# Kernel tuning notes

Measured on AMD Instinct MI355X. Metric: run time of the kernel, lower is better.

The kernel has to match this reference:

```python
import jax, jax.numpy as jnp
import numpy as np

NUM_HEADS = 16

def _apply_rope(t, cos, sin):
    # t: [B, nh, S, hd]; cos/sin: [S, hd//2]
    t1 = t[..., 0::2]
    t2 = t[..., 1::2]
    c = cos[None, None, :, :]
    s = sin[None, None, :, :]
    r1 = t1 * c - t2 * s
    r2 = t1 * s + t2 * c
    # interleave back to [..., hd]
    out = jnp.stack([r1, r2], axis=-1)
    return out.reshape(t.shape)

def setup_inputs() -> dict:
    key = jax.random.key(0)
    ks = jax.random.split(key, 6)
    B, S, H = 1, 4096, 1024
    hd = H // NUM_HEADS
    x = jax.random.normal(ks[0], (B, S, H), dtype=jnp.float32)
    # RoPE angle matrix: theta[pos, i] = pos / 10000^(2i/hd), shape [context, hd//2]
    pos = jnp.arange(S, dtype=jnp.float32)[:, None]
    inv_freq = 1.0 / (10000.0 ** (jnp.arange(0, hd, 2, dtype=jnp.float32) / hd))
    rotation = pos * inv_freq[None, :]
    sc = 1.0 / np.sqrt(H)
    W_qkv = jax.random.normal(ks[1], (H, 3 * H), dtype=jnp.float32) * sc
    b_qkv = jax.random.normal(ks[2], (3 * H,), dtype=jnp.float32) * 0.01
    W_out = jax.random.normal(ks[3], (H, H), dtype=jnp.float32) * sc
    b_out = jax.random.normal(ks[4], (H,), dtype=jnp.float32) * 0.01
    return {"x": x, "rotation": rotation, "W_qkv": W_qkv, "b_qkv": b_qkv,
            "W_out": W_out, "b_out": b_out, "window_size": 33}

def reference(x, rotation, W_qkv, b_qkv, W_out, b_out, window_size):
    B, S, H = x.shape
    nh = NUM_HEADS
    hd = H // nh
    W = window_size
    pad = W // 2
    qkv = x @ W_qkv + b_qkv                               # [B, S, 3H]
    qkv = qkv.reshape(B, S, nh, 3 * hd).transpose(0, 2, 1, 3)  # [B, nh, S, 3hd]
    q, k, v = jnp.split(qkv, 3, axis=-1)                  # each [B, nh, S, hd]
    cos = jnp.cos(rotation[:S])
    sin = jnp.sin(rotation[:S])
    q = _apply_rope(q, cos, sin)
    k = _apply_rope(k, cos, sin)
    # zero-pad along sequence, then gather sliding windows
    k_pad = jnp.pad(k, ((0, 0), (0, 0), (pad, pad), (0, 0)))
    v_pad = jnp.pad(v, ((0, 0), (0, 0), (pad, pad), (0, 0)))
    idx = jnp.arange(S)[:, None] + jnp.arange(W)[None, :]  # [S, W]
    k_win = k_pad[:, :, idx, :]                            # [B, nh, S, W, hd]
    v_win = v_pad[:, :, idx, :]
    scores = jnp.einsum('bnsh,bnswh->bnsw', q, k_win) / np.sqrt(hd)
    attn = jax.nn.softmax(scores, axis=-1)
    ctx = jnp.einsum('bnsw,bnswh->bnsh', attn, v_win)      # [B, nh, S, hd]
    ctx = ctx.transpose(0, 2, 1, 3).reshape(B, S, H)
    return ctx @ W_out + b_out
```

## Files before the change

kernel.cpp:

```cpp
#include <hip/hip_runtime.h>
#include <hip/hip_bf16.h>

#define S_LEN 4096
#define NH 16
#define HD 64
#define WIN 33
#define PAD 16
#define QT 64
#define KROWS 96
#define KPITCH_U 36

typedef short short8 __attribute__((ext_vector_type(8)));
typedef float f32x4 __attribute__((ext_vector_type(4)));

__device__ __forceinline__ float bl(unsigned u){ return __uint_as_float(u << 16); }
__device__ __forceinline__ float bh(unsigned u){ return __uint_as_float(u & 0xffff0000u); }
__device__ __forceinline__ unsigned f2bfu(float f){
  unsigned u = __float_as_uint(f);
  return (u + 0x7fffu + ((u >> 16) & 1u)) >> 16;
}
__device__ __forceinline__ unsigned pack2(float a, float b){ return f2bfu(a) | (f2bfu(b) << 16); }

__device__ __forceinline__ void gload_lds16(const void* g, void* l){
  __builtin_amdgcn_global_load_lds(
      (const __attribute__((address_space(1))) void*)g,
      (__attribute__((address_space(3))) void*)l, 16, 0, 0);
}


__global__ __launch_bounds__(256) void prep_all(
    const float* __restrict__ rot, float2* __restrict__ csq,
    const float* __restrict__ x, __hip_bfloat16* __restrict__ xb,
    const float* __restrict__ Wq, __hip_bfloat16* __restrict__ Wt1,
    const float* __restrict__ Wo, __hip_bfloat16* __restrict__ Wt2)
{
  __shared__ float tile[32][33];
  const int b = blockIdx.x, tid = threadIdx.x;
  if (b < 512) {
    int t = b * 256 + tid;
    float v = rot[t], sv, cv;
    __sincosf(v, &sv, &cv);
    csq[t] = make_float2(cv, sv);
  } else if (b < 2560) {
    int t = (b - 512) * 256 + tid;
    const float4* p = (const float4*)x + (size_t)t * 2;
    float4 a = p[0], c = p[1];
    uint4 o;
    o.x = pack2(a.x, a.y); o.y = pack2(a.z, a.w);
    o.z = pack2(c.x, c.y); o.w = pack2(c.z, c.w);
    ((uint4*)xb)[t] = o;
  } else {
    const float* in; unsigned short* out; int R, C, bx, by;
    if (b < 5632) { int bb = b - 2560; in = Wq; out = (unsigned short*)Wt1; R = 1024; C = 3072; bx = bb % 96; by = bb / 96; }
    else          { int bb = b - 5632; in = Wo; out = (unsigned short*)Wt2; R = 1024; C = 1024; bx = bb % 32; by = bb / 32; }
    int c0 = bx * 32, r0 = by * 32;
    int tx = tid & 31, ty = tid >> 5;
    #pragma unroll
    for (int i = 0; i < 4; ++i) {
      int r = ty + i * 8;
      tile[r][tx] = in[(size_t)(r0 + r) * C + c0 + tx];
    }
    __syncthreads();
    #pragma unroll
    for (int i = 0; i < 4; ++i) {
      int cc = ty + i * 8;
      out[(size_t)(c0 + cc) * R + r0 + tx] = (unsigned short)f2bfu(tile[tx][cc]);
    }
  }
}


__global__ __launch_bounds__(256, 4) void gemm_qkv_rope(
    const __hip_bfloat16* __restrict__ A,
    const __hip_bfloat16* __restrict__ Bt,
    const float* __restrict__ bias,
    const float2* __restrict__ csq,
    unsigned short* __restrict__ Cout,
    int M, int N, int K)
{
  __shared__ unsigned int lA[128 * 64 / 2];
  __shared__ unsigned int lB[96 * 64 / 2];
  const int tid = threadIdx.x;
  const int wave = tid >> 6, lane = tid & 63;
  const int m0 = blockIdx.y * 128, n0 = blockIdx.x * 96;
  const int wm = (wave >> 1) * 64, wn = (wave & 1) * 48;
  const int l16 = lane >> 4, l15 = lane & 15;

  f32x4 acc[4][3];
  #pragma unroll
  for (int i = 0; i < 4; ++i)
    #pragma unroll
    for (int j = 0; j < 3; ++j) acc[i][j] = (f32x4){0.f, 0.f, 0.f, 0.f};

  const int nkt = K / 64;
  for (int kt = 0; kt < nkt; ++kt) {
    __syncthreads();
    #pragma unroll
    for (int it = 0; it < 4; ++it) {
      const int c = it * 256 + tid;
      const int r = c >> 3, s8 = c & 7;
      const int ss = s8 ^ (r & 7);
      gload_lds16(A + (size_t)(m0 + r) * K + kt * 64 + ss * 8, (char*)lA + c * 16);
    }
    #pragma unroll
    for (int it = 0; it < 3; ++it) {
      const int c = it * 256 + tid;
      const int r = c >> 3, s8 = c & 7;
      const int ss = s8 ^ (r & 7);
      gload_lds16(Bt + (size_t)(n0 + r) * K + kt * 64 + ss * 8, (char*)lB + c * 16);
    }
    __syncthreads();
    #pragma unroll
    for (int ks = 0; ks < 2; ++ks) {
      short8 af[4], bfr[3];
      #pragma unroll
      for (int mi = 0; mi < 4; ++mi) {
        const int r = wm + mi * 16 + l15;
        const int slot = (ks * 4 + l16) ^ (r & 7);
        uint4 u = *(const uint4*)((const char*)lA + r * 128 + slot * 16);
        af[mi] = __builtin_bit_cast(short8, u);
      }
      #pragma unroll
      for (int ni = 0; ni < 3; ++ni) {
        const int r = wn + ni * 16 + l15;
        const int slot = (ks * 4 + l16) ^ (r & 7);
        uint4 u = *(const uint4*)((const char*)lB + r * 128 + slot * 16);
        bfr[ni] = __builtin_bit_cast(short8, u);
      }
      #pragma unroll
      for (int mi = 0; mi < 4; ++mi)
        #pragma unroll
        for (int ni = 0; ni < 3; ++ni)
          acc[mi][ni] = __builtin_amdgcn_mfma_f32_16x16x32_bf16(af[mi], bfr[ni], acc[mi][ni], 0, 0, 0);
    }
  }

  #pragma unroll
  for (int ni = 0; ni < 3; ++ni) {
    const int cn = n0 + wn + ni * 16 + l15;
    const int rseg = cn % 192;
    const float bv = bias[cn];
    if (rseg < 128) {
      const int i = (rseg & 63) >> 1;
      const float sgn = (cn & 1) ? 1.f : -1.f;
      #pragma unroll
      for (int mi = 0; mi < 4; ++mi) {
        #pragma unroll
        for (int j = 0; j < 4; ++j) {
          const int rm = m0 + wm + mi * 16 + l16 * 4 + j;
          const float v = acc[mi][ni][j] + bv;
          const float p = __shfl_xor(v, 1);
          const float2 cs = csq[rm * 32 + i];
          Cout[(size_t)rm * N + cn] = (unsigned short)f2bfu(v * cs.x + p * (sgn * cs.y));
        }
      }
    } else {
      #pragma unroll
      for (int mi = 0; mi < 4; ++mi) {
        #pragma unroll
        for (int j = 0; j < 4; ++j) {
          const int rm = m0 + wm + mi * 16 + l16 * 4 + j;
          Cout[(size_t)rm * N + cn] = (unsigned short)f2bfu(acc[mi][ni][j] + bv);
        }
      }
    }
  }
}


__global__ __launch_bounds__(256) void gemm_out(
    const __hip_bfloat16* __restrict__ A,
    const __hip_bfloat16* __restrict__ Bt,
    const float* __restrict__ bias,
    float* __restrict__ Cout,
    int M, int N, int K)
{
  __shared__ unsigned int lA[2][128 * 64 / 2];
  __shared__ unsigned int lB[2][64 * 64 / 2];
  const int tid = threadIdx.x;
  const int wave = tid >> 6, lane = tid & 63;
  const int m0 = blockIdx.y * 128, n0 = blockIdx.x * 64;
  const int wm = (wave >> 1) * 64, wn = (wave & 1) * 32;
  const int l16 = lane >> 4, l15 = lane & 15;

  f32x4 acc[4][2];
  #pragma unroll
  for (int i = 0; i < 4; ++i)
    #pragma unroll
    for (int j = 0; j < 2; ++j) acc[i][j] = (f32x4){0.f, 0.f, 0.f, 0.f};

  auto stage = [&](int buf, int kt) {
    #pragma unroll
    for (int it = 0; it < 4; ++it) {
      const int c = it * 256 + wave * 64 + lane;
      const int r = c >> 3, s8 = c & 7;
      const int ss = s8 ^ (r & 7);
      gload_lds16(A + (size_t)(m0 + r) * K + kt * 64 + ss * 8,
                  (char*)lA[buf] + (it * 256 + wave * 64) * 16);
    }
    #pragma unroll
    for (int it = 0; it < 2; ++it) {
      const int c = it * 256 + wave * 64 + lane;
      const int r = c >> 3, s8 = c & 7;
      const int ss = s8 ^ (r & 7);
      gload_lds16(Bt + (size_t)(n0 + r) * K + kt * 64 + ss * 8,
                  (char*)lB[buf] + (it * 256 + wave * 64) * 16);
    }
  };

  const int nkt = K / 64;
  stage(0, 0);
  int cur = 0;
  for (int kt = 0; kt < nkt; ++kt) {
    const bool pf = (kt + 1 < nkt);
    if (pf) stage(cur ^ 1, kt + 1);
    if (pf) asm volatile("s_waitcnt vmcnt(6)" ::: "memory");
    else    asm volatile("s_waitcnt vmcnt(0)" ::: "memory");
    __builtin_amdgcn_s_barrier();
    __builtin_amdgcn_sched_barrier(0);
    #pragma unroll
    for (int ks = 0; ks < 2; ++ks) {
      short8 af[4], bfr[2];
      #pragma unroll
      for (int mi = 0; mi < 4; ++mi) {
        const int r = wm + mi * 16 + l15;
        const int slot = (ks * 4 + l16) ^ (r & 7);
        uint4 u = *(const uint4*)((const char*)lA[cur] + r * 128 + slot * 16);
        af[mi] = __builtin_bit_cast(short8, u);
      }
      #pragma unroll
      for (int ni = 0; ni < 2; ++ni) {
        const int r = wn + ni * 16 + l15;
        const int slot = (ks * 4 + l16) ^ (r & 7);
        uint4 u = *(const uint4*)((const char*)lB[cur] + r * 128 + slot * 16);
        bfr[ni] = __builtin_bit_cast(short8, u);
      }
      __builtin_amdgcn_s_setprio(1);
      #pragma unroll
      for (int mi = 0; mi < 4; ++mi)
        #pragma unroll
        for (int ni = 0; ni < 2; ++ni)
          acc[mi][ni] = __builtin_amdgcn_mfma_f32_16x16x32_bf16(af[mi], bfr[ni], acc[mi][ni], 0, 0, 0);
      __builtin_amdgcn_s_setprio(0);
    }
    __builtin_amdgcn_sched_barrier(0);
    __builtin_amdgcn_s_barrier();
    cur ^= 1;
  }

  #pragma unroll
  for (int ni = 0; ni < 2; ++ni) {
    const int cn = n0 + wn + ni * 16 + l15;
    const float bv = bias[cn];
    #pragma unroll
    for (int mi = 0; mi < 4; ++mi) {
      #pragma unroll
      for (int j = 0; j < 4; ++j) {
        const int rm = m0 + wm + mi * 16 + l16 * 4 + j;
        Cout[(size_t)rm * N + cn] = acc[mi][ni][j] + bv;
      }
    }
  }
}


__global__ __launch_bounds__(256) void attn_kernel(const __hip_bfloat16* __restrict__ qkv,
                                                   __hip_bfloat16* __restrict__ ctx){
  __shared__ unsigned int kbuf[KROWS * KPITCH_U];
  __shared__ unsigned int vbuf[KROWS * KPITCH_U];
  const int tid = threadIdx.x;
  const int h   = blockIdx.x & 15;
  const int qs0 = (blockIdx.x >> 4) * QT;

  #pragma unroll
  for (int it = 0; it < 3; ++it) {
    int c = tid + it * 256;
    int r = c >> 3, s8 = c & 7;
    int srow = qs0 - PAD + r;
    uint4 kv = make_uint4(0, 0, 0, 0), vv = make_uint4(0, 0, 0, 0);
    if ((unsigned)srow < (unsigned)S_LEN) {
      kv = ((const uint4*)(qkv + (size_t)srow * 3072 + h * 192 + 64))[s8];
      vv = ((const uint4*)(qkv + (size_t)srow * 3072 + h * 192 + 128))[s8];
    }
    *(uint4*)(kbuf + r * KPITCH_U + s8 * 4) = kv;
    *(uint4*)(vbuf + r * KPITCH_U + s8 * 4) = vv;
  }

  const int ql = tid >> 2, t4 = tid & 3;
  const uint4* qp = (const uint4*)(qkv + (size_t)(qs0 + ql) * 3072 + h * 192);
  float qf[64];
  #pragma unroll
  for (int c = 0; c < 8; ++c) {
    uint4 v = qp[c];
    qf[c*8+0] = bl(v.x); qf[c*8+1] = bh(v.x);
    qf[c*8+2] = bl(v.y); qf[c*8+3] = bh(v.y);
    qf[c*8+4] = bl(v.z); qf[c*8+5] = bh(v.z);
    qf[c*8+6] = bl(v.w); qf[c*8+7] = bh(v.w);
  }
  __syncthreads();

  float sc[9];
  #pragma unroll
  for (int j = 0; j < 9; ++j) sc[j] = 0.f;
  float mx = -1e30f;
  #pragma unroll
  for (int j = 0; j < 9; ++j) {
    int w = t4 + 4 * j;
    if (w < WIN) {
      int rw = ql + w;
      const uint4* kp = (const uint4*)(kbuf + rw * KPITCH_U);
      float d = 0.f;
      #pragma unroll
      for (int c = 0; c < 8; ++c) {
        uint4 kv = kp[c];
        d += qf[c*8+0]*bl(kv.x) + qf[c*8+1]*bh(kv.x)
           + qf[c*8+2]*bl(kv.y) + qf[c*8+3]*bh(kv.y)
           + qf[c*8+4]*bl(kv.z) + qf[c*8+5]*bh(kv.z)
           + qf[c*8+6]*bl(kv.w) + qf[c*8+7]*bh(kv.w);
      }
      sc[j] = d * 0.125f;
      mx = fmaxf(mx, sc[j]);
    }
  }
  mx = fmaxf(mx, __shfl_xor(mx, 1));
  mx = fmaxf(mx, __shfl_xor(mx, 2));
  float sum = 0.f;
  #pragma unroll
  for (int j = 0; j < 9; ++j) {
    int w = t4 + 4 * j;
    if (w < WIN) { sc[j] = __expf(sc[j] - mx); sum += sc[j]; }
  }
  sum += __shfl_xor(sum, 1);
  sum += __shfl_xor(sum, 2);
  const float inv = 1.0f / sum;
  #pragma unroll
  for (int j = 0; j < 9; ++j) sc[j] *= inv;

  float accd[16];
  #pragma unroll
  for (int i = 0; i < 16; ++i) accd[i] = 0.f;
  #pragma unroll
  for (int w = 0; w < WIN; ++w) {
    float wgt = __shfl(sc[w >> 2], ((tid & 63) & ~3) | (w & 3), 64);
    int rw = ql + w;
    const uint4* vp = (const uint4*)(vbuf + rw * KPITCH_U + t4 * 8);
    uint4 a = vp[0], b = vp[1];
    float vf[16];
    vf[0]=bl(a.x); vf[1]=bh(a.x); vf[2]=bl(a.y); vf[3]=bh(a.y);
    vf[4]=bl(a.z); vf[5]=bh(a.z); vf[6]=bl(a.w); vf[7]=bh(a.w);
    vf[8]=bl(b.x); vf[9]=bh(b.x); vf[10]=bl(b.y); vf[11]=bh(b.y);
    vf[12]=bl(b.z); vf[13]=bh(b.z); vf[14]=bl(b.w); vf[15]=bh(b.w);
    #pragma unroll
    for (int i = 0; i < 16; ++i) accd[i] += wgt * vf[i];
  }

  unsigned short* op = (unsigned short*)ctx + (size_t)(qs0 + ql) * 1024 + h * 64 + t4 * 16;
  uint4 o1, o2;
  o1.x = pack2(accd[0], accd[1]);  o1.y = pack2(accd[2], accd[3]);
  o1.z = pack2(accd[4], accd[5]);  o1.w = pack2(accd[6], accd[7]);
  o2.x = pack2(accd[8], accd[9]);  o2.y = pack2(accd[10], accd[11]);
  o2.z = pack2(accd[12], accd[13]); o2.w = pack2(accd[14], accd[15]);
  *(uint4*)op = o1;
  *((uint4*)op + 1) = o2;
}


extern "C" void kernel_launch(void* const* d_in, const int* in_sizes, int n_in,
                              void* d_out, int out_size, void* d_ws, size_t ws_size,
                              hipStream_t stream)
{
  const float* x     = (const float*)d_in[0];
  const float* rot   = (const float*)d_in[1];
  const float* W_qkv = (const float*)d_in[2];
  const float* b_qkv = (const float*)d_in[3];
  const float* W_out = (const float*)d_in[4];
  const float* b_out = (const float*)d_in[5];
  float* out = (float*)d_out;

  char* ws = (char*)d_ws;
  __hip_bfloat16* xb   = (__hip_bfloat16*)(ws + 0);
  __hip_bfloat16* Wt1  = (__hip_bfloat16*)(ws + 8388608);
  __hip_bfloat16* Wt2  = (__hip_bfloat16*)(ws + 14680064);
  __hip_bfloat16* qkvb = (__hip_bfloat16*)(ws + 16777216);
  __hip_bfloat16* ctx  = (__hip_bfloat16*)(ws + 41943040);
  float2* csq          = (float2*)(ws + 50331648);

  prep_all<<<6656, 256, 0, stream>>>(rot, csq, x, xb, W_qkv, Wt1, W_out, Wt2);
  gemm_qkv_rope<<<dim3(3072 / 96, 4096 / 128), 256, 0, stream>>>(xb, Wt1, b_qkv, csq,
                                                                 (unsigned short*)qkvb, 4096, 3072, 1024);
  attn_kernel<<<64 * 16, 256, 0, stream>>>(qkvb, ctx);
  gemm_out<<<dim3(1024 / 64, 4096 / 128), 256, 0, stream>>>(ctx, Wt2, b_out, out, 4096, 1024, 1024);
}
```

Measured before the change: 87.95 us.

## Split-K output GEMM with atomic accumulation and bias prefill in prep kernel

The output projection GEMM now splits K in two across a third grid dimension, doubling block count from 512 to 1024, and accumulates partial results into the output with float atomicAdd. The bias is written into the output buffer beforehand by extra blocks in the prep kernel. To fit higher occupancy the LDS double-buffering and priority hints are removed in favour of a simple single-buffer loop. Atomics add memory traffic and make the summation order nondeterministic, and the dropped prefetch may expose load latency.

```diff
diff --git a/kernel.cpp b/kernel.cpp
--- a/kernel.cpp
+++ b/kernel.cpp
@@ -32,7 +32,8 @@
     const float* __restrict__ rot, float2* __restrict__ csq,
     const float* __restrict__ x, __hip_bfloat16* __restrict__ xb,
     const float* __restrict__ Wq, __hip_bfloat16* __restrict__ Wt1,
-    const float* __restrict__ Wo, __hip_bfloat16* __restrict__ Wt2)
+    const float* __restrict__ Wo, __hip_bfloat16* __restrict__ Wt2,
+    const float* __restrict__ b_out, float* __restrict__ out)
 {
   __shared__ float tile[32][33];
   const int b = blockIdx.x, tid = threadIdx.x;
@@ -49,10 +50,10 @@
     o.x = pack2(a.x, a.y); o.y = pack2(a.z, a.w);
     o.z = pack2(c.x, c.y); o.w = pack2(c.z, c.w);
     ((uint4*)xb)[t] = o;
-  } else {
-    const float* in; unsigned short* out; int R, C, bx, by;
-    if (b < 5632) { int bb = b - 2560; in = Wq; out = (unsigned short*)Wt1; R = 1024; C = 3072; bx = bb % 96; by = bb / 96; }
-    else          { int bb = b - 5632; in = Wo; out = (unsigned short*)Wt2; R = 1024; C = 1024; bx = bb % 32; by = bb / 32; }
+  } else if (b < 6656) {
+    const float* in; unsigned short* outp; int R, C, bx, by;
+    if (b < 5632) { int bb = b - 2560; in = Wq; outp = (unsigned short*)Wt1; R = 1024; C = 3072; bx = bb % 96; by = bb / 96; }
+    else          { int bb = b - 5632; in = Wo; outp = (unsigned short*)Wt2; R = 1024; C = 1024; bx = bb % 32; by = bb / 32; }
     int c0 = bx * 32, r0 = by * 32;
     int tx = tid & 31, ty = tid >> 5;
     #pragma unroll
@@ -64,8 +65,12 @@
     #pragma unroll
     for (int i = 0; i < 4; ++i) {
       int cc = ty + i * 8;
-      out[(size_t)(c0 + cc) * R + r0 + tx] = (unsigned short)f2bfu(tile[tx][cc]);
-    }
+      outp[(size_t)(c0 + cc) * R + r0 + tx] = (unsigned short)f2bfu(tile[tx][cc]);
+    }
+  } else {
+    int t = (b - 6656) * 256 + tid;
+    const int cn = (t * 4) & 1023;
+    ((float4*)out)[t] = *(const float4*)(b_out + cn);
   }
 }
 
@@ -168,18 +173,18 @@
 }
 
 
-__global__ __launch_bounds__(256) void gemm_out(
+__global__ __launch_bounds__(256, 4) void gemm_out_split(
     const __hip_bfloat16* __restrict__ A,
     const __hip_bfloat16* __restrict__ Bt,
-    const float* __restrict__ bias,
     float* __restrict__ Cout,
     int M, int N, int K)
 {
-  __shared__ unsigned int lA[2][128 * 64 / 2];
-  __shared__ unsigned int lB[2][64 * 64 / 2];
+  __shared__ unsigned int lA[128 * 64 / 2];
+  __shared__ unsigned int lB[64 * 64 / 2];
   const int tid = threadIdx.x;
   const int wave = tid >> 6, lane = tid & 63;
   const int m0 = blockIdx.y * 128, n0 = blockIdx.x * 64;
+  const int k0 = blockIdx.z * (K >> 1);
   const int wm = (wave >> 1) * 64, wn = (wave & 1) * 32;
   const int l16 = lane >> 4, l15 = lane & 15;
 
@@ -189,35 +194,24 @@
     #pragma unroll
     for (int j = 0; j < 2; ++j) acc[i][j] = (f32x4){0.f, 0.f, 0.f, 0.f};
 
-  auto stage = [&](int buf, int kt) {
+  const int nkt = (K >> 1) / 64;
+  for (int kt = 0; kt < nkt; ++kt) {
+    __syncthreads();
     #pragma unroll
     for (int it = 0; it < 4; ++it) {
-      const int c = it * 256 + wave * 64 + lane;
+      const int c = it * 256 + tid;
       const int r = c >> 3, s8 = c & 7;
       const int ss = s8 ^ (r & 7);
-      gload_lds16(A + (size_t)(m0 + r) * K + kt * 64 + ss * 8,
-                  (char*)lA[buf] + (it * 256 + wave * 64) * 16);
+      gload_lds16(A + (size_t)(m0 + r) * K + k0 + kt * 64 + ss * 8, (char*)lA + c * 16);
     }
     #pragma unroll
     for (int it = 0; it < 2; ++it) {
-      const int c = it * 256 + wave * 64 + lane;
+      const int c = it * 256 + tid;
       const int r = c >> 3, s8 = c & 7;
       const int ss = s8 ^ (r & 7);
-      gload_lds16(Bt + (size_t)(n0 + r) * K + kt * 64 + ss * 8,
-                  (char*)lB[buf] + (it * 256 + wave * 64) * 16);
-    }
-  };
-
-  const int nkt = K / 64;
-  stage(0, 0);
-  int cur = 0;
-  for (int kt = 0; kt < nkt; ++kt) {
-    const bool pf = (kt + 1 < nkt);
-    if (pf) stage(cur ^ 1, kt + 1);
-    if (pf) asm volatile("s_waitcnt vmcnt(6)" ::: "memory");
-    else    asm volatile("s_waitcnt vmcnt(0)" ::: "memory");
-    __builtin_amdgcn_s_barrier();
-    __builtin_amdgcn_sched_barrier(0);
+      gload_lds16(Bt + (size_t)(n0 + r) * K + k0 + kt * 64 + ss * 8, (char*)lB + c * 16);
+    }
+    __syncthreads();
     #pragma unroll
     for (int ks = 0; ks < 2; ++ks) {
       short8 af[4], bfr[2];
@@ -225,39 +219,33 @@
       for (int mi = 0; mi < 4; ++mi) {
         const int r = wm + mi * 16 + l15;
         const int slot = (ks * 4 + l16) ^ (r & 7);
-        uint4 u = *(const uint4*)((const char*)lA[cur] + r * 128 + slot * 16);
+        uint4 u = *(const uint4*)((const char*)lA + r * 128 + slot * 16);
         af[mi] = __builtin_bit_cast(short8, u);
       }
       #pragma unroll
       for (int ni = 0; ni < 2; ++ni) {
         const int r = wn + ni * 16 + l15;
         const int slot = (ks * 4 + l16) ^ (r & 7);
-        uint4 u = *(const uint4*)((const char*)lB[cur] + r * 128 + slot * 16);
+        uint4 u = *(const uint4*)((const char*)lB + r * 128 + slot * 16);
         bfr[ni] = __builtin_bit_cast(short8, u);
       }
-      __builtin_amdgcn_s_setprio(1);
       #pragma unroll
       for (int mi = 0; mi < 4; ++mi)
         #pragma unroll
         for (int ni = 0; ni < 2; ++ni)
           acc[mi][ni] = __builtin_amdgcn_mfma_f32_16x16x32_bf16(af[mi], bfr[ni], acc[mi][ni], 0, 0, 0);
-      __builtin_amdgcn_s_setprio(0);
-    }
-    __builtin_amdgcn_sched_barrier(0);
-    __builtin_amdgcn_s_barrier();
-    cur ^= 1;
+    }
   }
 
   #pragma unroll
   for (int ni = 0; ni < 2; ++ni) {
     const int cn = n0 + wn + ni * 16 + l15;
-    const float bv = bias[cn];
     #pragma unroll
     for (int mi = 0; mi < 4; ++mi) {
       #pragma unroll
       for (int j = 0; j < 4; ++j) {
         const int rm = m0 + wm + mi * 16 + l16 * 4 + j;
-        Cout[(size_t)rm * N + cn] = acc[mi][ni][j] + bv;
+        atomicAdd(&Cout[(size_t)rm * N + cn], acc[mi][ni][j]);
       }
     }
   }
@@ -385,9 +373,9 @@
   __hip_bfloat16* ctx  = (__hip_bfloat16*)(ws + 41943040);
   float2* csq          = (float2*)(ws + 50331648);
 
-  prep_all<<<6656, 256, 0, stream>>>(rot, csq, x, xb, W_qkv, Wt1, W_out, Wt2);
+  prep_all<<<10752, 256, 0, stream>>>(rot, csq, x, xb, W_qkv, Wt1, W_out, Wt2, b_out, out);
   gemm_qkv_rope<<<dim3(3072 / 96, 4096 / 128), 256, 0, stream>>>(xb, Wt1, b_qkv, csq,
                                                                  (unsigned short*)qkvb, 4096, 3072, 1024);
   attn_kernel<<<64 * 16, 256, 0, stream>>>(qkvb, ctx);
-  gemm_out<<<dim3(1024 / 64, 4096 / 128), 256, 0, stream>>>(ctx, Wt2, b_out, out, 4096, 1024, 1024);
-}
+  gemm_out_split<<<dim3(1024 / 64, 4096 / 128, 2), 256, 0, stream>>>(ctx, Wt2, out, 4096, 1024, 1024);
+}
```

New measurement: 106.9 us. 1.22x slower.
